# Kernel optimization log

Measured on AMD Instinct MI355X. Metric: run time of the kernel, lower is better.

The kernel has to match this reference:

```python
import jax, jax.numpy as jnp
import numpy as np

N = 262144
D = 6
M = 6
EPS = 1e-05
ALPHA = 0.05


def _w(k, out_dim, in_dim):
    # Kaiming-uniform-ish init like torch Linear default
    bound = 1.0 / np.sqrt(in_dim)
    return jax.random.uniform(k, (out_dim, in_dim), jnp.float32, -bound, bound)


def _b(k, out_dim, in_dim):
    bound = 1.0 / np.sqrt(in_dim)
    return jax.random.uniform(k, (out_dim,), jnp.float32, -bound, bound)


def setup_inputs() -> dict:
    key = jax.random.key(0)
    ks = jax.random.split(key, 32)
    inp = {
        "X": jax.random.normal(ks[0], (N, D), jnp.float32),
        "U": jax.random.normal(ks[1], (N, M), jnp.float32),
        "xref": jax.random.normal(ks[2], (1, D), jnp.float32),
        # FNN: 6 -> 80 -> 200 -> 6
        "fnn_w1": _w(ks[3], 80, D), "fnn_b1": _b(ks[4], 80, D),
        "fnn_w2": _w(ks[5], 200, 80), "fnn_b2": _b(ks[6], 200, 80),
        "fnn_w3": _w(ks[7], D, 200), "fnn_b3": _b(ks[8], D, 200),
        # GNN: 6 -> 36
        "gnn_w": _w(ks[9], D * M, D), "gnn_b": _b(ks[10], D * M, D),
        # ICNN: 6 -> 60 -> 60 -> 30 -> 1 with input skips
        "icnn_w1": _w(ks[11], 60, D), "icnn_b1": _b(ks[12], 60, D),
        "icnn_w2": _w(ks[13], 60, 60), "icnn_b2": _b(ks[14], 60, 60),
        "icnn_w3": _w(ks[15], 30, 60), "icnn_b3": _b(ks[16], 30, 60),
        "icnn_w4": _w(ks[17], 1, 30), "icnn_b4": _b(ks[18], 1, 30),
        "icnn_im2": _w(ks[19], 60, D),
        "icnn_im3": _w(ks[20], 30, D),
        "icnn_im4": _w(ks[21], 1, D),
    }
    return inp


def reference(X, U, xref,
              fnn_w1, fnn_b1, fnn_w2, fnn_b2, fnn_w3, fnn_b3,
              gnn_w, gnn_b,
              icnn_w1, icnn_b1, icnn_w2, icnn_b2, icnn_w3, icnn_b3,
              icnn_w4, icnn_b4, icnn_im2, icnn_im3, icnn_im4):
    def lin(x, W, b=None):
        y = x @ W.T
        return y if b is None else y + b

    def icnn(x):  # (n, D) -> (n, 1)
        h = jax.nn.softplus(lin(x, icnn_w1, icnn_b1))
        h = jax.nn.softplus(lin(h, icnn_w2, icnn_b2) + lin(x, icnn_im2))
        h = jax.nn.softplus(lin(h, icnn_w3, icnn_b3) + lin(x, icnn_im3))
        return lin(h, icnn_w4, icnn_b4) + lin(x, icnn_im4)

    def V_fn(Xb):  # (n, D) -> (n,)
        h = icnn(Xb)[:, 0] - icnn(xref)[0, 0]
        # sigma(h) = (h>=1)(h-0.5) + (0<h<1)(0.5 h^2)
        sigma = jnp.where(h >= 1.0, h - 0.5,
                          jnp.where(h > 0.0, 0.5 * h * h, 0.0))
        dx = Xb - xref
        return sigma + EPS * jnp.sum(dx * dx, axis=1)

    # FNN (tanh hiddens)
    h = jnp.tanh(lin(X, fnn_w1, fnn_b1))
    h = jnp.tanh(lin(h, fnn_w2, fnn_b2))
    f_X = lin(h, fnn_w3, fnn_b3)  # (N, D)

    # GNN
    g_X = lin(X, gnn_w, gnn_b).reshape(X.shape[0], D, M)  # (N, D, M)

    # Lyapunov value and its gradient (per-sample, via grad of summed V)
    V = V_fn(X)  # (N,)
    dV = jax.grad(lambda Z: jnp.sum(V_fn(Z)))(X)  # (N, D)

    # Stability correction
    sc = jnp.sum(dV * f_X, axis=1) + ALPHA * V
    sc = sc - jnp.sum(jnp.abs(jnp.einsum('nd,ndm->nm', dV, g_X)), axis=1)
    dV_norm = dV / jnp.sum(dV * dV, axis=1, keepdims=True)
    f_cor = -dV_norm * jax.nn.relu(sc)[:, None]

    dX_opt = f_X + f_cor + jnp.einsum('ndm,nm->nd', g_X, U)
    return dX_opt
```

## Files before the change

kernel.cpp:

```cpp
#include <hip/hip_runtime.h>

#define EPS 1e-05f
#define ALPHA 0.05f

typedef _Float16 h2v __attribute__((ext_vector_type(2)));
typedef _Float16 f16x8 __attribute__((ext_vector_type(8)));
typedef float f32x16 __attribute__((ext_vector_type(16)));

__device__ __forceinline__ float rcp_f(float x){ return __builtin_amdgcn_rcpf(x); }
__device__ __forceinline__ float dot2(h2v a, h2v b, float c){
  return __builtin_amdgcn_fdot2(a, b, c, false);
}
__device__ __forceinline__ h2v uh(uint u){ return __builtin_bit_cast(h2v, u); }
__device__ __forceinline__ float uf(uint u){ return __builtin_bit_cast(float, u); }

#define LOG2E 1.4426950408889634f
#define LN2   0.6931471805599453f

__device__ __forceinline__ float fast_tanh(float x){
  float ax = fabsf(x);
  float e  = exp2f(ax * (-2.0f * LOG2E));
  float t  = (1.0f - e) * rcp_f(1.0f + e);
  return copysignf(t, x);
}
__device__ __forceinline__ float fast_sp(float x){
  float ax = fabsf(x);
  float e  = exp2f(ax * -LOG2E);
  return fmaxf(x, 0.0f) + log2f(1.0f + e) * LN2;
}
__device__ __forceinline__ float fast_sig(float x){
  float ax = fabsf(x);
  float e  = exp2f(ax * -LOG2E);
  float r  = rcp_f(1.0f + e);
  return x >= 0.0f ? r : e * r;
}
__device__ __forceinline__ float sig_from_sp(float sp){
  return 1.0f - exp2f(sp * -LOG2E);
}
__device__ __forceinline__ h2v mkh2(float a, float b){
  h2v r; r.x = (_Float16)a; r.y = (_Float16)b; return r;
}
__device__ __forceinline__ uint packh(float a, float b){
  ushort lo = __builtin_bit_cast(ushort, (_Float16)a);
  ushort hi = __builtin_bit_cast(ushort, (_Float16)b);
  return (uint)lo | ((uint)hi << 16);
}

__global__ __launch_bounds__(512, 2) void holo_main(
    const float* __restrict__ X, const float* __restrict__ U,
    const float* __restrict__ xref,
    const float* __restrict__ fw1, const float* __restrict__ fb1,
    const float* __restrict__ fw2, const float* __restrict__ fb2,
    const float* __restrict__ fw3, const float* __restrict__ fb3,
    const float* __restrict__ gw,  const float* __restrict__ gb,
    const float* __restrict__ iw1, const float* __restrict__ ib1,
    const float* __restrict__ iw2, const float* __restrict__ ib2,
    const float* __restrict__ iw3, const float* __restrict__ ib3,
    const float* __restrict__ iw4, const float* __restrict__ ib4,
    const float* __restrict__ im2, const float* __restrict__ im3,
    const float* __restrict__ im4,
    float* __restrict__ out, int N)
{
  __shared__ alignas(16) ushort sW2r[224*84];
  __shared__ uint4 sW3E[224];
  __shared__ uint4 sPW1B[80];
  __shared__ uint4 sPGB[36];
  __shared__ uint4 sPI1B[60];
  __shared__ uint4 sPI1C[60];
  __shared__ uint4 sPI3[240];
  __shared__ uint4 sPI3C[240];
  __shared__ uint4 sPM2B[60];
  __shared__ uint4 sPM2C[60];
  __shared__ uint4 sPM3B[60];
  __shared__ uint4 sPM3C[30];
  __shared__ uint  sPM4u[4];
  __shared__ alignas(16) uint sPI2Tu[1800];
  __shared__ uint4 sPI2C[480];
  __shared__ float sFB3[6], sXREF[6], sIM4[6];
  __shared__ float sS1[60], sS2[60], sS3[30];
  __shared__ float sYREF, sIB4;

  const int t = threadIdx.x;
  const int T = 512;
  const int lane = t & 63;

  for (int idx=t; idx<224*42; idx+=T){
    int row = idx/42, c = idx%42, k = 2*c;
    uint v = 0;
    if (row < 200 && k < 80) v = packh(fw2[row*80+k], fw2[row*80+k+1]);
    ((uint*)sW2r)[idx] = v;
  }
  for (int idx=t; idx<896; idx+=T){
    int P = idx/8, c = idx%8, n = 2*P;
    uint v = 0;
    if (n < 200){
      if (c < 6)       v = packh(fw3[c*200+n], fw3[c*200+n+1]);
      else if (c == 6) v = __builtin_bit_cast(uint, fb2[n]);
      else             v = __builtin_bit_cast(uint, fb2[n+1]);
    }
    ((uint*)sW3E)[idx] = v;
  }
  for (int idx=t; idx<320; idx+=T){
    int o = idx/4, c = idx%4;
    ((uint*)sPW1B)[idx] = (c<3) ? packh(fw1[o*6+2*c], fw1[o*6+2*c+1])
                                : __builtin_bit_cast(uint, fb1[o]);
  }
  for (int idx=t; idx<144; idx+=T){
    int o = idx/4, c = idx%4;
    ((uint*)sPGB)[idx] = (c<3) ? packh(gw[o*6+2*c], gw[o*6+2*c+1])
                               : __builtin_bit_cast(uint, gb[o]);
  }
  for (int idx=t; idx<240; idx+=T){
    int p = idx/8, c = idx%8, sub = c/4, cc = c%4, nr = 2*p+sub;
    ((uint*)sPI1B)[idx] = (cc<3) ? packh(iw1[nr*6+2*cc], iw1[nr*6+2*cc+1])
                                 : __builtin_bit_cast(uint, ib1[nr]);
  }
  for (int idx=t; idx<240; idx+=T){
    int q = idx/8, c = idx%8;
    ((uint*)sPI1C)[idx] = (c<6) ? packh(iw1[(2*q)*6+c], iw1[(2*q+1)*6+c]) : 0u;
  }
  for (int idx=t; idx<960; idx+=T){
    int r = idx/32, q = idx%32;
    ((uint*)sPI3)[idx] = (q<30) ? packh(iw3[r*60+2*q], iw3[r*60+2*q+1]) : 0u;
  }
  for (int idx=t; idx<960; idx+=T){
    int j = idx/16, q = idx%16;
    ((uint*)sPI3C)[idx] = (q<15) ? packh(iw3[(2*q)*60+j], iw3[(2*q+1)*60+j]) : 0u;
  }
  for (int idx=t; idx<240; idx+=T){
    int j = idx/4, c = idx%4;
    ((uint*)sPM2B)[idx] = (c<3) ? packh(im2[j*6+2*c], im2[j*6+2*c+1])
                                : __builtin_bit_cast(uint, ib2[j]);
  }
  for (int idx=t; idx<240; idx+=T){
    int q = idx/8, c = idx%8;
    ((uint*)sPM2C)[idx] = (c<6) ? packh(im2[(2*q)*6+c], im2[(2*q+1)*6+c]) : 0u;
  }
  for (int idx=t; idx<240; idx+=T){
    int r = idx/8, c = idx%8;
    uint v = 0;
    if (c < 3)       v = packh(im3[r*6+2*c], im3[r*6+2*c+1]);
    else if (c == 3) v = __builtin_bit_cast(uint, ib3[r]);
    else if (c == 4) v = __builtin_bit_cast(uint, iw4[r]);
    ((uint*)sPM3B)[idx] = v;
  }
  for (int idx=t; idx<120; idx+=T){
    int q = idx/8, c = idx%8;
    ((uint*)sPM3C)[idx] = (c<6) ? packh(im3[(2*q)*6+c], im3[(2*q+1)*6+c]) : 0u;
  }
  for (int idx=t; idx<4; idx+=T)
    sPM4u[idx] = (idx<3) ? packh(im4[2*idx], im4[2*idx+1]) : 0u;
  for (int idx=t; idx<1800; idx+=T){
    int p = idx/60, j = idx%60;
    sPI2Tu[idx] = packh(iw2[j*60+2*p], iw2[j*60+2*p+1]);
  }
  for (int idx=t; idx<1920; idx+=T){
    int k1 = idx/32, q = idx%32;
    ((uint*)sPI2C)[idx] = (q<30) ? packh(iw2[(2*q)*60+k1], iw2[(2*q+1)*60+k1]) : 0u;
  }
  for (int k=t;k<6;k+=T){ sFB3[k]=fb3[k]; sIM4[k]=im4[k]; sXREF[k]=xref[k]; }
  if (t==0) sIB4=ib4[0];
  __syncthreads();

  {
    h2v xrp[3];
    #pragma unroll
    for (int p = 0; p < 3; p++) xrp[p] = mkh2(sXREF[2*p], sXREF[2*p+1]);
    if (t < 60){
      const uint* w = (const uint*)sPI1B + (t/2)*8 + (t&1)*4;
      float z = uf(w[3]);
      #pragma unroll
      for (int c = 0; c < 3; c++) z = dot2(uh(w[c]), xrp[c], z);
      sS1[t] = fast_sp(z);
    }
    __syncthreads();
    if (t < 60){
      const uint* m = (const uint*)sPM2B + t*4;
      float z = uf(m[3]);
      #pragma unroll
      for (int c = 0; c < 3; c++) z = dot2(uh(m[c]), xrp[c], z);
      for (int p = 0; p < 30; p++)
        z = dot2(uh(sPI2Tu[p*60+t]), mkh2(sS1[2*p], sS1[2*p+1]), z);
      sS2[t] = fast_sp(z);
    }
    __syncthreads();
    if (t < 30){
      const uint* m = (const uint*)sPM3B + t*8;
      float z = uf(m[3]);
      #pragma unroll
      for (int c = 0; c < 3; c++) z = dot2(uh(m[c]), xrp[c], z);
      const uint* prow = (const uint*)sPI3 + t*32;
      for (int q = 0; q < 30; q++)
        z = dot2(uh(prow[q]), mkh2(sS2[2*q], sS2[2*q+1]), z);
      sS3[t] = fast_sp(z);
    }
    __syncthreads();
    if (t == 0){
      float y = sIB4;
      #pragma unroll
      for (int p = 0; p < 3; p++) y = dot2(uh(sPM4u[p]), xrp[p], y);
      for (int j = 0; j < 30; j++) y = fmaf(uf(((const uint*)sPM3B)[j*8+4]), sS3[j], y);
      sYREF = y;
    }
    __syncthreads();
  }

  const int i = blockIdx.x * blockDim.x + t;
  const bool valid = (i < N);

  float x[6]; h2v xp[3];
  #pragma unroll
  for (int k = 0; k < 6; k++) x[k] = valid ? X[(long)i*6 + k] : 0.0f;
  #pragma unroll
  for (int p = 0; p < 3; p++) xp[p] = mkh2(x[2*p], x[2*p+1]);

  uint h1u[40];
  #pragma unroll
  for (int o = 0; o < 80; o += 2){
    uint4 wa = sPW1B[o], wb = sPW1B[o+1];
    float z0 = uf(wa.w), z1 = uf(wb.w);
    z0 = dot2(uh(wa.x), xp[0], z0); z0 = dot2(uh(wa.y), xp[1], z0); z0 = dot2(uh(wa.z), xp[2], z0);
    z1 = dot2(uh(wb.x), xp[0], z1); z1 = dot2(uh(wb.y), xp[1], z1); z1 = dot2(uh(wb.z), xp[2], z1);
    h1u[o/2] = packh(fast_tanh(z0), fast_tanh(z1));
  }

  const int hh = lane >> 5;
  const int l31 = lane & 31;

  uint bf0[5][4], bf1[5][4];
  {
    int a0 = 4 * l31;
    int a1 = 4 * (32 + l31);
    #pragma unroll
    for (int kt = 0; kt < 5; kt++){
      #pragma unroll
      for (int q = 0; q < 4; q++){
        int lo0 = __builtin_amdgcn_ds_bpermute(a0, (int)h1u[kt*8 + q]);
        int hi0 = __builtin_amdgcn_ds_bpermute(a0, (int)h1u[kt*8 + 4 + q]);
        bf0[kt][q] = hh ? (uint)hi0 : (uint)lo0;
        int lo1 = __builtin_amdgcn_ds_bpermute(a1, (int)h1u[kt*8 + q]);
        int hi1 = __builtin_amdgcn_ds_bpermute(a1, (int)h1u[kt*8 + 4 + q]);
        bf1[kt][q] = hh ? (uint)hi1 : (uint)lo1;
      }
    }
  }

  float fp0[6] = {0.f,0.f,0.f,0.f,0.f,0.f};
  float fp1[6] = {0.f,0.f,0.f,0.f,0.f,0.f};
  for (int mt = 0; mt < 7; mt++){
    const int row = mt*32 + l31;
    f16x8 af[5];
    #pragma unroll
    for (int kt = 0; kt < 5; kt++){
      const ushort* wp = &sW2r[row*84 + kt*16 + 8*hh];
      uint2 w0 = *(const uint2*)wp;
      uint2 w1 = *(const uint2*)(wp + 4);
      uint4 au; au.x = w0.x; au.y = w0.y; au.z = w1.x; au.w = w1.y;
      af[kt] = __builtin_bit_cast(f16x8, au);
    }
    f32x16 acc0 = {0,0,0,0,0,0,0,0,0,0,0,0,0,0,0,0};
    f32x16 acc1 = {0,0,0,0,0,0,0,0,0,0,0,0,0,0,0,0};
    #pragma unroll
    for (int kt = 0; kt < 5; kt++){
      uint4 b0u; b0u.x=bf0[kt][0]; b0u.y=bf0[kt][1]; b0u.z=bf0[kt][2]; b0u.w=bf0[kt][3];
      uint4 b1u; b1u.x=bf1[kt][0]; b1u.y=bf1[kt][1]; b1u.z=bf1[kt][2]; b1u.w=bf1[kt][3];
      acc0 = __builtin_amdgcn_mfma_f32_32x32x16_f16(af[kt], __builtin_bit_cast(f16x8, b0u), acc0, 0, 0, 0);
      acc1 = __builtin_amdgcn_mfma_f32_32x32x16_f16(af[kt], __builtin_bit_cast(f16x8, b1u), acc1, 0, 0, 0);
    }
    #pragma unroll
    for (int c = 0; c < 4; c++){
      #pragma unroll
      for (int b0h = 0; b0h < 2; b0h++){
        const int r0 = 4*c + 2*b0h;
        const int P  = mt*16 + 4*c + 2*hh + b0h;
        uint4 wa = sW3E[P*2], wb = sW3E[P*2+1];
        float bA = uf(wb.z), bB = uf(wb.w);
        h2v tp0 = mkh2(fast_tanh(acc0[r0] + bA), fast_tanh(acc0[r0+1] + bB));
        h2v tp1 = mkh2(fast_tanh(acc1[r0] + bA), fast_tanh(acc1[r0+1] + bB));
        fp0[0] = dot2(uh(wa.x), tp0, fp0[0]); fp1[0] = dot2(uh(wa.x), tp1, fp1[0]);
        fp0[1] = dot2(uh(wa.y), tp0, fp0[1]); fp1[1] = dot2(uh(wa.y), tp1, fp1[1]);
        fp0[2] = dot2(uh(wa.z), tp0, fp0[2]); fp1[2] = dot2(uh(wa.z), tp1, fp1[2]);
        fp0[3] = dot2(uh(wa.w), tp0, fp0[3]); fp1[3] = dot2(uh(wa.w), tp1, fp1[3]);
        fp0[4] = dot2(uh(wb.x), tp0, fp0[4]); fp1[4] = dot2(uh(wb.x), tp1, fp1[4]);
        fp0[5] = dot2(uh(wb.y), tp0, fp0[5]); fp1[5] = dot2(uh(wb.y), tp1, fp1[5]);
      }
    }
  }
  float f[6];
  #pragma unroll
  for (int d = 0; d < 6; d++){
    float s0 = fp0[d] + __shfl_xor(fp0[d], 32, 64);
    float s1 = fp1[d] + __shfl_xor(fp1[d], 32, 64);
    f[d] = sFB3[d] + (hh ? s1 : s0);
  }

  float c2[60];
  #pragma unroll
  for (int j = 0; j < 60; j++){
    uint4 m = sPM2B[j];
    float z = uf(m.w);
    z = dot2(uh(m.x), xp[0], z); z = dot2(uh(m.y), xp[1], z); z = dot2(uh(m.z), xp[2], z);
    c2[j] = z;
  }
  for (int p = 0; p < 30; p++){
    uint4 wA = sPI1B[2*p], wB = sPI1B[2*p+1];
    float za = uf(wA.w), zb = uf(wB.w);
    za = dot2(uh(wA.x), xp[0], za); za = dot2(uh(wA.y), xp[1], za); za = dot2(uh(wA.z), xp[2], za);
    zb = dot2(uh(wB.x), xp[0], zb); zb = dot2(uh(wB.y), xp[1], zb); zb = dot2(uh(wB.z), xp[2], zb);
    h2v s = mkh2(fast_sp(za), fast_sp(zb));
    const uint* rowp = sPI2Tu + p*60;
    #pragma unroll
    for (int jj = 0; jj < 15; jj++){
      uint4 v = *(const uint4*)(rowp + jj*4);
      c2[4*jj+0] = dot2(uh(v.x), s, c2[4*jj+0]);
      c2[4*jj+1] = dot2(uh(v.y), s, c2[4*jj+1]);
      c2[4*jj+2] = dot2(uh(v.z), s, c2[4*jj+2]);
      c2[4*jj+3] = dot2(uh(v.w), s, c2[4*jj+3]);
    }
  }
  h2v c2p[32];
  #pragma unroll
  for (int j = 0; j < 60; j += 2)
    c2p[j/2] = mkh2(fast_sp(c2[j]), fast_sp(c2[j+1]));
  c2p[30] = mkh2(0.f, 0.f); c2p[31] = mkh2(0.f, 0.f);

  float y = sIB4;
  #pragma unroll
  for (int p = 0; p < 3; p++) y = dot2(uh(sPM4u[p]), xp[p], y);
  float ac[6];
  #pragma unroll
  for (int d = 0; d < 6; d++) ac[d] = sIM4[d];
  float g3[30];
  #pragma unroll
  for (int i3 = 0; i3 < 30; i3++){
    uint4 m0 = sPM3B[2*i3], m1 = sPM3B[2*i3+1];
    float z = uf(m0.w);
    z = dot2(uh(m0.x), xp[0], z); z = dot2(uh(m0.y), xp[1], z); z = dot2(uh(m0.z), xp[2], z);
    const uint4* prow = sPI3 + i3*8;
    #pragma unroll
    for (int q4 = 0; q4 < 8; q4++){
      uint4 v = prow[q4];
      z = dot2(uh(v.x), c2p[4*q4+0], z);
      z = dot2(uh(v.y), c2p[4*q4+1], z);
      z = dot2(uh(v.z), c2p[4*q4+2], z);
      z = dot2(uh(v.w), c2p[4*q4+3], z);
    }
    float sp3 = fast_sp(z);
    float w4  = uf(m1.x);
    y = fmaf(w4, sp3, y);
    g3[i3] = w4 * sig_from_sp(sp3);
  }
  h2v g3p[16];
  #pragma unroll
  for (int q = 0; q < 15; q++) g3p[q] = mkh2(g3[2*q], g3[2*q+1]);
  g3p[15] = mkh2(0.f, 0.f);
  #pragma unroll
  for (int q = 0; q < 15; q++){
    uint4 a = sPM3C[2*q], b = sPM3C[2*q+1];
    ac[0] = dot2(uh(a.x), g3p[q], ac[0]);
    ac[1] = dot2(uh(a.y), g3p[q], ac[1]);
    ac[2] = dot2(uh(a.z), g3p[q], ac[2]);
    ac[3] = dot2(uh(a.w), g3p[q], ac[3]);
    ac[4] = dot2(uh(b.x), g3p[q], ac[4]);
    ac[5] = dot2(uh(b.y), g3p[q], ac[5]);
  }

  h2v g2p[32];
  #pragma unroll
  for (int jp = 0; jp < 30; jp++){
    const uint4* r0p = sPI3C + (2*jp)*4;
    const uint4* r1p = sPI3C + (2*jp+1)*4;
    float ta = 0.0f, tb = 0.0f;
    #pragma unroll
    for (int q4 = 0; q4 < 4; q4++){
      uint4 v0 = r0p[q4], v1 = r1p[q4];
      ta = dot2(uh(v0.x), g3p[4*q4+0], ta);
      ta = dot2(uh(v0.y), g3p[4*q4+1], ta);
      ta = dot2(uh(v0.z), g3p[4*q4+2], ta);
      ta = dot2(uh(v0.w), g3p[4*q4+3], ta);
      tb = dot2(uh(v1.x), g3p[4*q4+0], tb);
      tb = dot2(uh(v1.y), g3p[4*q4+1], tb);
      tb = dot2(uh(v1.z), g3p[4*q4+2], tb);
      tb = dot2(uh(v1.w), g3p[4*q4+3], tb);
    }
    h2v sp = c2p[jp];
    ta *= sig_from_sp((float)sp.x);
    tb *= sig_from_sp((float)sp.y);
    h2v tp = mkh2(ta, tb);
    g2p[jp] = tp;
    uint4 a = sPM2C[2*jp], b = sPM2C[2*jp+1];
    ac[0] = dot2(uh(a.x), tp, ac[0]);
    ac[1] = dot2(uh(a.y), tp, ac[1]);
    ac[2] = dot2(uh(a.z), tp, ac[2]);
    ac[3] = dot2(uh(a.w), tp, ac[3]);
    ac[4] = dot2(uh(b.x), tp, ac[4]);
    ac[5] = dot2(uh(b.y), tp, ac[5]);
  }
  g2p[30] = mkh2(0.f, 0.f); g2p[31] = mkh2(0.f, 0.f);

  for (int p = 0; p < 30; p++){
    uint4 wA = sPI1B[2*p], wB = sPI1B[2*p+1];
    float za = uf(wA.w), zb = uf(wB.w);
    za = dot2(uh(wA.x), xp[0], za); za = dot2(uh(wA.y), xp[1], za); za = dot2(uh(wA.z), xp[2], za);
    zb = dot2(uh(wB.x), xp[0], zb); zb = dot2(uh(wB.y), xp[1], zb); zb = dot2(uh(wB.z), xp[2], zb);
    const uint4* c0 = sPI2C + (2*p)*8;
    const uint4* c1 = sPI2C + (2*p+1)*8;
    float ta = 0.0f, tb = 0.0f;
    #pragma unroll
    for (int q4 = 0; q4 < 8; q4++){
      uint4 v0 = c0[q4], v1 = c1[q4];
      ta = dot2(uh(v0.x), g2p[4*q4+0], ta);
      ta = dot2(uh(v0.y), g2p[4*q4+1], ta);
      ta = dot2(uh(v0.z), g2p[4*q4+2], ta);
      ta = dot2(uh(v0.w), g2p[4*q4+3], ta);
      tb = dot2(uh(v1.x), g2p[4*q4+0], tb);
      tb = dot2(uh(v1.y), g2p[4*q4+1], tb);
      tb = dot2(uh(v1.z), g2p[4*q4+2], tb);
      tb = dot2(uh(v1.w), g2p[4*q4+3], tb);
    }
    ta *= fast_sig(za); tb *= fast_sig(zb);
    h2v tp = mkh2(ta, tb);
    uint4 a = sPI1C[2*p], b = sPI1C[2*p+1];
    ac[0] = dot2(uh(a.x), tp, ac[0]);
    ac[1] = dot2(uh(a.y), tp, ac[1]);
    ac[2] = dot2(uh(a.z), tp, ac[2]);
    ac[3] = dot2(uh(a.w), tp, ac[3]);
    ac[4] = dot2(uh(b.x), tp, ac[4]);
    ac[5] = dot2(uh(b.y), tp, ac[5]);
  }

  float hdiff = y - sYREF;
  float sigma = (hdiff >= 1.0f) ? (hdiff - 0.5f) : ((hdiff > 0.0f) ? 0.5f*hdiff*hdiff : 0.0f);
  float sigp  = (hdiff >= 1.0f) ? 1.0f          : ((hdiff > 0.0f) ? hdiff             : 0.0f);
  float dx2 = 0.0f;
  float dV[6];
  #pragma unroll
  for (int d = 0; d < 6; d++){
    float dx = x[d] - sXREF[d];
    dx2 = fmaf(dx, dx, dx2);
    dV[d] = fmaf(sigp, ac[d], 2.0f*EPS*dx);
  }
  float V = sigma + EPS*dx2;

  float sc = ALPHA * V;
  #pragma unroll
  for (int d = 0; d < 6; d++) sc = fmaf(dV[d], f[d], sc);

  float u[6];
  #pragma unroll
  for (int m = 0; m < 6; m++) u[m] = valid ? U[(long)i*6 + m] : 0.0f;
  float am[6] = {0.f,0.f,0.f,0.f,0.f,0.f};
  float gU[6];
  #pragma unroll
  for (int d = 0; d < 6; d++){
    float acc = 0.0f;
    #pragma unroll
    for (int m = 0; m < 6; m++){
      int o = d*6 + m;
      uint4 g4 = sPGB[o];
      float g = uf(g4.w);
      g = dot2(uh(g4.x), xp[0], g); g = dot2(uh(g4.y), xp[1], g); g = dot2(uh(g4.z), xp[2], g);
      am[m] = fmaf(dV[d], g, am[m]);
      acc   = fmaf(g, u[m], acc);
    }
    gU[d] = acc;
  }
  #pragma unroll
  for (int m = 0; m < 6; m++) sc -= fabsf(am[m]);

  float n2 = 0.0f;
  #pragma unroll
  for (int d = 0; d < 6; d++) n2 = fmaf(dV[d], dV[d], n2);
  float r = fmaxf(sc, 0.0f) * rcp_f(n2);

  if (valid){
    #pragma unroll
    for (int d = 0; d < 6; d++)
      out[(long)i*6 + d] = f[d] - dV[d]*r + gU[d];
  }
}

extern "C" void kernel_launch(void* const* d_in, const int* in_sizes, int n_in,
                              void* d_out, int out_size, void* d_ws, size_t ws_size,
                              hipStream_t stream)
{
  const float* X    = (const float*)d_in[0];
  const float* U    = (const float*)d_in[1];
  const float* xref = (const float*)d_in[2];
  const float* fw1  = (const float*)d_in[3];
  const float* fb1  = (const float*)d_in[4];
  const float* fw2  = (const float*)d_in[5];
  const float* fb2  = (const float*)d_in[6];
  const float* fw3  = (const float*)d_in[7];
  const float* fb3  = (const float*)d_in[8];
  const float* gw   = (const float*)d_in[9];
  const float* gb   = (const float*)d_in[10];
  const float* iw1  = (const float*)d_in[11];
  const float* ib1  = (const float*)d_in[12];
  const float* iw2  = (const float*)d_in[13];
  const float* ib2  = (const float*)d_in[14];
  const float* iw3  = (const float*)d_in[15];
  const float* ib3  = (const float*)d_in[16];
  const float* iw4  = (const float*)d_in[17];
  const float* ib4  = (const float*)d_in[18];
  const float* im2  = (const float*)d_in[19];
  const float* im3  = (const float*)d_in[20];
  const float* im4  = (const float*)d_in[21];

  float* out = (float*)d_out;
  int N = in_sizes[0] / 6;

  int threads = 512;
  int blocks  = (N + threads - 1) / threads;
  holo_main<<<blocks, threads, 0, stream>>>(X, U, xref,
      fw1, fb1, fw2, fb2, fw3, fb3, gw, gb,
      iw1, ib1, iw2, ib2, iw3, ib3, iw4, ib4, im2, im3, im4,
      out, N);
}
```

Before: 198.3 us.

## Move packed ICNN/GNN weights to constant memory via a prep kernel

Adds a single-block prep kernel that packs most small weight tables and computes the xref ICNN value once, then copies them device-to-device into a __constant__ buffer. The main kernel reads these uniform weights from constant memory (scalar loads) instead of staging them into LDS in every block. This removes per-block global loads, packing and barriers, and shrinks LDS use. The cost is an extra kernel launch, a memcpy on the stream, and more scalar-load pressure and register use in the main kernel. It also skips a few dead W3 iterations.

```diff
diff --git a/kernel.cpp b/kernel.cpp
--- a/kernel.cpp
+++ b/kernel.cpp
@@ -46,43 +46,168 @@
   return (uint)lo | ((uint)hi << 16);
 }
 
-__global__ __launch_bounds__(512, 2) void holo_main(
-    const float* __restrict__ X, const float* __restrict__ U,
+static constexpr int O_PW1B = 0;
+static constexpr int O_PGB  = 320;
+static constexpr int O_PI1B = 464;
+static constexpr int O_PI1C = 704;
+static constexpr int O_PI3  = 944;
+static constexpr int O_PI3C = 1904;
+static constexpr int O_PM2B = 2928;
+static constexpr int O_PM2C = 3184;
+static constexpr int O_PM3B = 3440;
+static constexpr int O_PM3C = 3680;
+static constexpr int O_PM4  = 3800;
+static constexpr int O_FB3  = 3804;
+static constexpr int O_XREF = 3810;
+static constexpr int O_IM4  = 3816;
+static constexpr int O_IB4  = 3822;
+static constexpr int O_YREF = 3823;
+static constexpr int O_PI2T = 3824;
+static constexpr int O_PI2C = 5624;
+static constexpr int W_TOTAL = 7544;
+
+__device__ uint g_stage[W_TOTAL];
+__constant__ uint cW[W_TOTAL];
+
+__global__ void holo_prep(
     const float* __restrict__ xref,
     const float* __restrict__ fw1, const float* __restrict__ fb1,
-    const float* __restrict__ fw2, const float* __restrict__ fb2,
-    const float* __restrict__ fw3, const float* __restrict__ fb3,
+    const float* __restrict__ fb3,
     const float* __restrict__ gw,  const float* __restrict__ gb,
     const float* __restrict__ iw1, const float* __restrict__ ib1,
     const float* __restrict__ iw2, const float* __restrict__ ib2,
     const float* __restrict__ iw3, const float* __restrict__ ib3,
     const float* __restrict__ iw4, const float* __restrict__ ib4,
     const float* __restrict__ im2, const float* __restrict__ im3,
-    const float* __restrict__ im4,
+    const float* __restrict__ im4)
+{
+  uint* gs = g_stage;
+  const int t = threadIdx.x, T = 256;
+  __shared__ float sS1[60], sS2[60], sS3[30];
+
+  for (int idx=t; idx<320; idx+=T){
+    int o = idx/4, c = idx%4;
+    gs[O_PW1B+idx] = (c<3) ? packh(fw1[o*6+2*c], fw1[o*6+2*c+1])
+                           : __builtin_bit_cast(uint, fb1[o]);
+  }
+  for (int idx=t; idx<144; idx+=T){
+    int o = idx/4, c = idx%4;
+    gs[O_PGB+idx] = (c<3) ? packh(gw[o*6+2*c], gw[o*6+2*c+1])
+                          : __builtin_bit_cast(uint, gb[o]);
+  }
+  for (int idx=t; idx<240; idx+=T){
+    int p = idx/8, c = idx%8, sub = c/4, cc = c%4, nr = 2*p+sub;
+    gs[O_PI1B+idx] = (cc<3) ? packh(iw1[nr*6+2*cc], iw1[nr*6+2*cc+1])
+                            : __builtin_bit_cast(uint, ib1[nr]);
+  }
+  for (int idx=t; idx<240; idx+=T){
+    int q = idx/8, c = idx%8;
+    gs[O_PI1C+idx] = (c<6) ? packh(iw1[(2*q)*6+c], iw1[(2*q+1)*6+c]) : 0u;
+  }
+  for (int idx=t; idx<960; idx+=T){
+    int r = idx/32, q = idx%32;
+    gs[O_PI3+idx] = (q<30) ? packh(iw3[r*60+2*q], iw3[r*60+2*q+1]) : 0u;
+  }
+  for (int idx=t; idx<1024; idx+=T){
+    int j = idx/16, q = idx%16;
+    gs[O_PI3C+idx] = (j<60 && q<15) ? packh(iw3[(2*q)*60+j], iw3[(2*q+1)*60+j]) : 0u;
+  }
+  for (int idx=t; idx<256; idx+=T){
+    int j = idx/4, c = idx%4;
+    uint v = 0;
+    if (j < 60) v = (c<3) ? packh(im2[j*6+2*c], im2[j*6+2*c+1])
+                          : __builtin_bit_cast(uint, ib2[j]);
+    gs[O_PM2B+idx] = v;
+  }
+  for (int idx=t; idx<256; idx+=T){
+    int q = idx/8, c = idx%8;
+    gs[O_PM2C+idx] = (q<30 && c<6) ? packh(im2[(2*q)*6+c], im2[(2*q+1)*6+c]) : 0u;
+  }
+  for (int idx=t; idx<240; idx+=T){
+    int r = idx/8, c = idx%8;
+    uint v = 0;
+    if (c < 3)       v = packh(im3[r*6+2*c], im3[r*6+2*c+1]);
+    else if (c == 3) v = __builtin_bit_cast(uint, ib3[r]);
+    else if (c == 4) v = __builtin_bit_cast(uint, iw4[r]);
+    gs[O_PM3B+idx] = v;
+  }
+  for (int idx=t; idx<120; idx+=T){
+    int q = idx/8, c = idx%8;
+    gs[O_PM3C+idx] = (c<6) ? packh(im3[(2*q)*6+c], im3[(2*q+1)*6+c]) : 0u;
+  }
+  for (int idx=t; idx<4; idx+=T)
+    gs[O_PM4+idx] = (idx<3) ? packh(im4[2*idx], im4[2*idx+1]) : 0u;
+  for (int k=t; k<6; k+=T){
+    gs[O_FB3+k]  = __builtin_bit_cast(uint, fb3[k]);
+    gs[O_XREF+k] = __builtin_bit_cast(uint, xref[k]);
+    gs[O_IM4+k]  = __builtin_bit_cast(uint, im4[k]);
+  }
+  if (t==0) gs[O_IB4] = __builtin_bit_cast(uint, ib4[0]);
+  for (int idx=t; idx<1800; idx+=T){
+    int p = idx/60, j = idx%60;
+    gs[O_PI2T+idx] = packh(iw2[j*60+2*p], iw2[j*60+2*p+1]);
+  }
+  for (int idx=t; idx<1920; idx+=T){
+    int k1 = idx/32, q = idx%32;
+    gs[O_PI2C+idx] = (q<30) ? packh(iw2[(2*q)*60+k1], iw2[(2*q+1)*60+k1]) : 0u;
+  }
+  __threadfence_block();
+  __syncthreads();
+
+  h2v xrp[3];
+  #pragma unroll
+  for (int p = 0; p < 3; p++) xrp[p] = mkh2(xref[2*p], xref[2*p+1]);
+  if (t < 60){
+    const uint* w = gs + O_PI1B + (t/2)*8 + (t&1)*4;
+    float z = uf(w[3]);
+    #pragma unroll
+    for (int c = 0; c < 3; c++) z = dot2(uh(w[c]), xrp[c], z);
+    sS1[t] = fast_sp(z);
+  }
+  __syncthreads();
+  if (t < 60){
+    const uint* m = gs + O_PM2B + t*4;
+    float z = uf(m[3]);
+    #pragma unroll
+    for (int c = 0; c < 3; c++) z = dot2(uh(m[c]), xrp[c], z);
+    for (int p = 0; p < 30; p++)
+      z = dot2(uh(gs[O_PI2T + p*60 + t]), mkh2(sS1[2*p], sS1[2*p+1]), z);
+    sS2[t] = fast_sp(z);
+  }
+  __syncthreads();
+  if (t < 30){
+    const uint* m = gs + O_PM3B + t*8;
+    float z = uf(m[3]);
+    #pragma unroll
+    for (int c = 0; c < 3; c++) z = dot2(uh(m[c]), xrp[c], z);
+    for (int q = 0; q < 30; q++)
+      z = dot2(uh(gs[O_PI3 + t*32 + q]), mkh2(sS2[2*q], sS2[2*q+1]), z);
+    sS3[t] = fast_sp(z);
+  }
+  __syncthreads();
+  if (t == 0){
+    float y = uf(gs[O_IB4]);
+    #pragma unroll
+    for (int p = 0; p < 3; p++) y = dot2(uh(gs[O_PM4+p]), xrp[p], y);
+    for (int j = 0; j < 30; j++) y = fmaf(uf(gs[O_PM3B+j*8+4]), sS3[j], y);
+    gs[O_YREF] = __builtin_bit_cast(uint, y);
+  }
+}
+
+__global__ __launch_bounds__(512, 2) void holo_main(
+    const float* __restrict__ X, const float* __restrict__ U,
+    const float* __restrict__ fw2, const float* __restrict__ fb2,
+    const float* __restrict__ fw3,
     float* __restrict__ out, int N)
 {
   __shared__ alignas(16) ushort sW2r[224*84];
   __shared__ uint4 sW3E[224];
-  __shared__ uint4 sPW1B[80];
-  __shared__ uint4 sPGB[36];
-  __shared__ uint4 sPI1B[60];
-  __shared__ uint4 sPI1C[60];
-  __shared__ uint4 sPI3[240];
-  __shared__ uint4 sPI3C[240];
-  __shared__ uint4 sPM2B[60];
-  __shared__ uint4 sPM2C[60];
-  __shared__ uint4 sPM3B[60];
-  __shared__ uint4 sPM3C[30];
-  __shared__ uint  sPM4u[4];
-  __shared__ alignas(16) uint sPI2Tu[1800];
-  __shared__ uint4 sPI2C[480];
-  __shared__ float sFB3[6], sXREF[6], sIM4[6];
-  __shared__ float sS1[60], sS2[60], sS3[30];
-  __shared__ float sYREF, sIB4;
 
   const int t = threadIdx.x;
   const int T = 512;
   const int lane = t & 63;
+  const int hh  = lane >> 5;
+  const int l31 = lane & 31;
 
   for (int idx=t; idx<224*42; idx+=T){
     int row = idx/42, c = idx%42, k = 2*c;
@@ -100,110 +225,7 @@
     }
     ((uint*)sW3E)[idx] = v;
   }
-  for (int idx=t; idx<320; idx+=T){
-    int o = idx/4, c = idx%4;
-    ((uint*)sPW1B)[idx] = (c<3) ? packh(fw1[o*6+2*c], fw1[o*6+2*c+1])
-                                : __builtin_bit_cast(uint, fb1[o]);
-  }
-  for (int idx=t; idx<144; idx+=T){
-    int o = idx/4, c = idx%4;
-    ((uint*)sPGB)[idx] = (c<3) ? packh(gw[o*6+2*c], gw[o*6+2*c+1])
-                               : __builtin_bit_cast(uint, gb[o]);
-  }
-  for (int idx=t; idx<240; idx+=T){
-    int p = idx/8, c = idx%8, sub = c/4, cc = c%4, nr = 2*p+sub;
-    ((uint*)sPI1B)[idx] = (cc<3) ? packh(iw1[nr*6+2*cc], iw1[nr*6+2*cc+1])
-                                 : __builtin_bit_cast(uint, ib1[nr]);
-  }
-  for (int idx=t; idx<240; idx+=T){
-    int q = idx/8, c = idx%8;
-    ((uint*)sPI1C)[idx] = (c<6) ? packh(iw1[(2*q)*6+c], iw1[(2*q+1)*6+c]) : 0u;
-  }
-  for (int idx=t; idx<960; idx+=T){
-    int r = idx/32, q = idx%32;
-    ((uint*)sPI3)[idx] = (q<30) ? packh(iw3[r*60+2*q], iw3[r*60+2*q+1]) : 0u;
-  }
-  for (int idx=t; idx<960; idx+=T){
-    int j = idx/16, q = idx%16;
-    ((uint*)sPI3C)[idx] = (q<15) ? packh(iw3[(2*q)*60+j], iw3[(2*q+1)*60+j]) : 0u;
-  }
-  for (int idx=t; idx<240; idx+=T){
-    int j = idx/4, c = idx%4;
-    ((uint*)sPM2B)[idx] = (c<3) ? packh(im2[j*6+2*c], im2[j*6+2*c+1])
-                                : __builtin_bit_cast(uint, ib2[j]);
-  }
-  for (int idx=t; idx<240; idx+=T){
-    int q = idx/8, c = idx%8;
-    ((uint*)sPM2C)[idx] = (c<6) ? packh(im2[(2*q)*6+c], im2[(2*q+1)*6+c]) : 0u;
-  }
-  for (int idx=t; idx<240; idx+=T){
-    int r = idx/8, c = idx%8;
-    uint v = 0;
-    if (c < 3)       v = packh(im3[r*6+2*c], im3[r*6+2*c+1]);
-    else if (c == 3) v = __builtin_bit_cast(uint, ib3[r]);
-    else if (c == 4) v = __builtin_bit_cast(uint, iw4[r]);
-    ((uint*)sPM3B)[idx] = v;
-  }
-  for (int idx=t; idx<120; idx+=T){
-    int q = idx/8, c = idx%8;
-    ((uint*)sPM3C)[idx] = (c<6) ? packh(im3[(2*q)*6+c], im3[(2*q+1)*6+c]) : 0u;
-  }
-  for (int idx=t; idx<4; idx+=T)
-    sPM4u[idx] = (idx<3) ? packh(im4[2*idx], im4[2*idx+1]) : 0u;
-  for (int idx=t; idx<1800; idx+=T){
-    int p = idx/60, j = idx%60;
-    sPI2Tu[idx] = packh(iw2[j*60+2*p], iw2[j*60+2*p+1]);
-  }
-  for (int idx=t; idx<1920; idx+=T){
-    int k1 = idx/32, q = idx%32;
-    ((uint*)sPI2C)[idx] = (q<30) ? packh(iw2[(2*q)*60+k1], iw2[(2*q+1)*60+k1]) : 0u;
-  }
-  for (int k=t;k<6;k+=T){ sFB3[k]=fb3[k]; sIM4[k]=im4[k]; sXREF[k]=xref[k]; }
-  if (t==0) sIB4=ib4[0];
   __syncthreads();
-
-  {
-    h2v xrp[3];
-    #pragma unroll
-    for (int p = 0; p < 3; p++) xrp[p] = mkh2(sXREF[2*p], sXREF[2*p+1]);
-    if (t < 60){
-      const uint* w = (const uint*)sPI1B + (t/2)*8 + (t&1)*4;
-      float z = uf(w[3]);
-      #pragma unroll
-      for (int c = 0; c < 3; c++) z = dot2(uh(w[c]), xrp[c], z);
-      sS1[t] = fast_sp(z);
-    }
-    __syncthreads();
-    if (t < 60){
-      const uint* m = (const uint*)sPM2B + t*4;
-      float z = uf(m[3]);
-      #pragma unroll
-      for (int c = 0; c < 3; c++) z = dot2(uh(m[c]), xrp[c], z);
-      for (int p = 0; p < 30; p++)
-        z = dot2(uh(sPI2Tu[p*60+t]), mkh2(sS1[2*p], sS1[2*p+1]), z);
-      sS2[t] = fast_sp(z);
-    }
-    __syncthreads();
-    if (t < 30){
-      const uint* m = (const uint*)sPM3B + t*8;
-      float z = uf(m[3]);
-      #pragma unroll
-      for (int c = 0; c < 3; c++) z = dot2(uh(m[c]), xrp[c], z);
-      const uint* prow = (const uint*)sPI3 + t*32;
-      for (int q = 0; q < 30; q++)
-        z = dot2(uh(prow[q]), mkh2(sS2[2*q], sS2[2*q+1]), z);
-      sS3[t] = fast_sp(z);
-    }
-    __syncthreads();
-    if (t == 0){
-      float y = sIB4;
-      #pragma unroll
-      for (int p = 0; p < 3; p++) y = dot2(uh(sPM4u[p]), xrp[p], y);
-      for (int j = 0; j < 30; j++) y = fmaf(uf(((const uint*)sPM3B)[j*8+4]), sS3[j], y);
-      sYREF = y;
-    }
-    __syncthreads();
-  }
 
   const int i = blockIdx.x * blockDim.x + t;
   const bool valid = (i < N);
@@ -217,15 +239,14 @@
   uint h1u[40];
   #pragma unroll
   for (int o = 0; o < 80; o += 2){
-    uint4 wa = sPW1B[o], wb = sPW1B[o+1];
-    float z0 = uf(wa.w), z1 = uf(wb.w);
-    z0 = dot2(uh(wa.x), xp[0], z0); z0 = dot2(uh(wa.y), xp[1], z0); z0 = dot2(uh(wa.z), xp[2], z0);
-    z1 = dot2(uh(wb.x), xp[0], z1); z1 = dot2(uh(wb.y), xp[1], z1); z1 = dot2(uh(wb.z), xp[2], z1);
+    float z0 = uf(cW[O_PW1B + o*4 + 3]), z1 = uf(cW[O_PW1B + (o+1)*4 + 3]);
+    #pragma unroll
+    for (int c = 0; c < 3; c++){
+      z0 = dot2(uh(cW[O_PW1B + o*4 + c]),     xp[c], z0);
+      z1 = dot2(uh(cW[O_PW1B + (o+1)*4 + c]), xp[c], z1);
+    }
     h1u[o/2] = packh(fast_tanh(z0), fast_tanh(z1));
   }
-
-  const int hh = lane >> 5;
-  const int l31 = lane & 31;
 
   uint bf0[5][4], bf1[5][4];
   {
@@ -271,6 +292,7 @@
     for (int c = 0; c < 4; c++){
       #pragma unroll
       for (int b0h = 0; b0h < 2; b0h++){
+        if (mt == 6 && c > 0) continue;
         const int r0 = 4*c + 2*b0h;
         const int P  = mt*16 + 4*c + 2*hh + b0h;
         uint4 wa = sW3E[P*2], wb = sW3E[P*2+1];
@@ -291,152 +313,114 @@
   for (int d = 0; d < 6; d++){
     float s0 = fp0[d] + __shfl_xor(fp0[d], 32, 64);
     float s1 = fp1[d] + __shfl_xor(fp1[d], 32, 64);
-    f[d] = sFB3[d] + (hh ? s1 : s0);
+    f[d] = uf(cW[O_FB3+d]) + (hh ? s1 : s0);
   }
 
   float c2[60];
   #pragma unroll
   for (int j = 0; j < 60; j++){
-    uint4 m = sPM2B[j];
-    float z = uf(m.w);
-    z = dot2(uh(m.x), xp[0], z); z = dot2(uh(m.y), xp[1], z); z = dot2(uh(m.z), xp[2], z);
+    float z = uf(cW[O_PM2B + j*4 + 3]);
+    z = dot2(uh(cW[O_PM2B+j*4+0]), xp[0], z);
+    z = dot2(uh(cW[O_PM2B+j*4+1]), xp[1], z);
+    z = dot2(uh(cW[O_PM2B+j*4+2]), xp[2], z);
     c2[j] = z;
   }
   for (int p = 0; p < 30; p++){
-    uint4 wA = sPI1B[2*p], wB = sPI1B[2*p+1];
-    float za = uf(wA.w), zb = uf(wB.w);
-    za = dot2(uh(wA.x), xp[0], za); za = dot2(uh(wA.y), xp[1], za); za = dot2(uh(wA.z), xp[2], za);
-    zb = dot2(uh(wB.x), xp[0], zb); zb = dot2(uh(wB.y), xp[1], zb); zb = dot2(uh(wB.z), xp[2], zb);
+    float za = uf(cW[O_PI1B + p*8 + 3]);
+    float zb = uf(cW[O_PI1B + p*8 + 7]);
+    #pragma unroll
+    for (int c = 0; c < 3; c++){
+      za = dot2(uh(cW[O_PI1B + p*8 + c]),     xp[c], za);
+      zb = dot2(uh(cW[O_PI1B + p*8 + 4 + c]), xp[c], zb);
+    }
     h2v s = mkh2(fast_sp(za), fast_sp(zb));
-    const uint* rowp = sPI2Tu + p*60;
-    #pragma unroll
-    for (int jj = 0; jj < 15; jj++){
-      uint4 v = *(const uint4*)(rowp + jj*4);
-      c2[4*jj+0] = dot2(uh(v.x), s, c2[4*jj+0]);
-      c2[4*jj+1] = dot2(uh(v.y), s, c2[4*jj+1]);
-      c2[4*jj+2] = dot2(uh(v.z), s, c2[4*jj+2]);
-      c2[4*jj+3] = dot2(uh(v.w), s, c2[4*jj+3]);
-    }
-  }
-  h2v c2p[32];
+    #pragma unroll
+    for (int j = 0; j < 60; j++)
+      c2[j] = dot2(uh(cW[O_PI2T + p*60 + j]), s, c2[j]);
+  }
+  h2v c2p[30];
   #pragma unroll
   for (int j = 0; j < 60; j += 2)
     c2p[j/2] = mkh2(fast_sp(c2[j]), fast_sp(c2[j+1]));
-  c2p[30] = mkh2(0.f, 0.f); c2p[31] = mkh2(0.f, 0.f);
-
-  float y = sIB4;
-  #pragma unroll
-  for (int p = 0; p < 3; p++) y = dot2(uh(sPM4u[p]), xp[p], y);
+
+  float y = uf(cW[O_IB4]);
+  #pragma unroll
+  for (int p = 0; p < 3; p++) y = dot2(uh(cW[O_PM4+p]), xp[p], y);
   float ac[6];
   #pragma unroll
-  for (int d = 0; d < 6; d++) ac[d] = sIM4[d];
-  float g3[30];
+  for (int d = 0; d < 6; d++) ac[d] = uf(cW[O_IM4+d]);
+  h2v g3p[15];
+  float g3even;
   #pragma unroll
   for (int i3 = 0; i3 < 30; i3++){
-    uint4 m0 = sPM3B[2*i3], m1 = sPM3B[2*i3+1];
-    float z = uf(m0.w);
-    z = dot2(uh(m0.x), xp[0], z); z = dot2(uh(m0.y), xp[1], z); z = dot2(uh(m0.z), xp[2], z);
-    const uint4* prow = sPI3 + i3*8;
-    #pragma unroll
-    for (int q4 = 0; q4 < 8; q4++){
-      uint4 v = prow[q4];
-      z = dot2(uh(v.x), c2p[4*q4+0], z);
-      z = dot2(uh(v.y), c2p[4*q4+1], z);
-      z = dot2(uh(v.z), c2p[4*q4+2], z);
-      z = dot2(uh(v.w), c2p[4*q4+3], z);
-    }
+    float z = uf(cW[O_PM3B + i3*8 + 3]);
+    z = dot2(uh(cW[O_PM3B+i3*8+0]), xp[0], z);
+    z = dot2(uh(cW[O_PM3B+i3*8+1]), xp[1], z);
+    z = dot2(uh(cW[O_PM3B+i3*8+2]), xp[2], z);
+    #pragma unroll
+    for (int q = 0; q < 30; q++)
+      z = dot2(uh(cW[O_PI3 + i3*32 + q]), c2p[q], z);
     float sp3 = fast_sp(z);
-    float w4  = uf(m1.x);
+    float w4  = uf(cW[O_PM3B + i3*8 + 4]);
     y = fmaf(w4, sp3, y);
-    g3[i3] = w4 * sig_from_sp(sp3);
-  }
-  h2v g3p[16];
-  #pragma unroll
-  for (int q = 0; q < 15; q++) g3p[q] = mkh2(g3[2*q], g3[2*q+1]);
-  g3p[15] = mkh2(0.f, 0.f);
+    float gi = w4 * sig_from_sp(sp3);
+    if (i3 & 1) g3p[i3>>1] = mkh2(g3even, gi); else g3even = gi;
+  }
   #pragma unroll
   for (int q = 0; q < 15; q++){
-    uint4 a = sPM3C[2*q], b = sPM3C[2*q+1];
-    ac[0] = dot2(uh(a.x), g3p[q], ac[0]);
-    ac[1] = dot2(uh(a.y), g3p[q], ac[1]);
-    ac[2] = dot2(uh(a.z), g3p[q], ac[2]);
-    ac[3] = dot2(uh(a.w), g3p[q], ac[3]);
-    ac[4] = dot2(uh(b.x), g3p[q], ac[4]);
-    ac[5] = dot2(uh(b.y), g3p[q], ac[5]);
-  }
-
-  h2v g2p[32];
+    #pragma unroll
+    for (int d = 0; d < 6; d++)
+      ac[d] = dot2(uh(cW[O_PM3C + q*8 + d]), g3p[q], ac[d]);
+  }
+
+  h2v g2p[30];
   #pragma unroll
   for (int jp = 0; jp < 30; jp++){
-    const uint4* r0p = sPI3C + (2*jp)*4;
-    const uint4* r1p = sPI3C + (2*jp+1)*4;
     float ta = 0.0f, tb = 0.0f;
     #pragma unroll
-    for (int q4 = 0; q4 < 4; q4++){
-      uint4 v0 = r0p[q4], v1 = r1p[q4];
-      ta = dot2(uh(v0.x), g3p[4*q4+0], ta);
-      ta = dot2(uh(v0.y), g3p[4*q4+1], ta);
-      ta = dot2(uh(v0.z), g3p[4*q4+2], ta);
-      ta = dot2(uh(v0.w), g3p[4*q4+3], ta);
-      tb = dot2(uh(v1.x), g3p[4*q4+0], tb);
-      tb = dot2(uh(v1.y), g3p[4*q4+1], tb);
-      tb = dot2(uh(v1.z), g3p[4*q4+2], tb);
-      tb = dot2(uh(v1.w), g3p[4*q4+3], tb);
+    for (int q = 0; q < 15; q++){
+      ta = dot2(uh(cW[O_PI3C + (2*jp)*16 + q]),   g3p[q], ta);
+      tb = dot2(uh(cW[O_PI3C + (2*jp+1)*16 + q]), g3p[q], tb);
     }
     h2v sp = c2p[jp];
     ta *= sig_from_sp((float)sp.x);
     tb *= sig_from_sp((float)sp.y);
     h2v tp = mkh2(ta, tb);
     g2p[jp] = tp;
-    uint4 a = sPM2C[2*jp], b = sPM2C[2*jp+1];
-    ac[0] = dot2(uh(a.x), tp, ac[0]);
-    ac[1] = dot2(uh(a.y), tp, ac[1]);
-    ac[2] = dot2(uh(a.z), tp, ac[2]);
-    ac[3] = dot2(uh(a.w), tp, ac[3]);
-    ac[4] = dot2(uh(b.x), tp, ac[4]);
-    ac[5] = dot2(uh(b.y), tp, ac[5]);
-  }
-  g2p[30] = mkh2(0.f, 0.f); g2p[31] = mkh2(0.f, 0.f);
+    #pragma unroll
+    for (int d = 0; d < 6; d++)
+      ac[d] = dot2(uh(cW[O_PM2C + jp*8 + d]), tp, ac[d]);
+  }
 
   for (int p = 0; p < 30; p++){
-    uint4 wA = sPI1B[2*p], wB = sPI1B[2*p+1];
-    float za = uf(wA.w), zb = uf(wB.w);
-    za = dot2(uh(wA.x), xp[0], za); za = dot2(uh(wA.y), xp[1], za); za = dot2(uh(wA.z), xp[2], za);
-    zb = dot2(uh(wB.x), xp[0], zb); zb = dot2(uh(wB.y), xp[1], zb); zb = dot2(uh(wB.z), xp[2], zb);
-    const uint4* c0 = sPI2C + (2*p)*8;
-    const uint4* c1 = sPI2C + (2*p+1)*8;
+    float za = uf(cW[O_PI1B + p*8 + 3]);
+    float zb = uf(cW[O_PI1B + p*8 + 7]);
+    #pragma unroll
+    for (int c = 0; c < 3; c++){
+      za = dot2(uh(cW[O_PI1B + p*8 + c]),     xp[c], za);
+      zb = dot2(uh(cW[O_PI1B + p*8 + 4 + c]), xp[c], zb);
+    }
     float ta = 0.0f, tb = 0.0f;
     #pragma unroll
-    for (int q4 = 0; q4 < 8; q4++){
-      uint4 v0 = c0[q4], v1 = c1[q4];
-      ta = dot2(uh(v0.x), g2p[4*q4+0], ta);
-      ta = dot2(uh(v0.y), g2p[4*q4+1], ta);
-      ta = dot2(uh(v0.z), g2p[4*q4+2], ta);
-      ta = dot2(uh(v0.w), g2p[4*q4+3], ta);
-      tb = dot2(uh(v1.x), g2p[4*q4+0], tb);
-      tb = dot2(uh(v1.y), g2p[4*q4+1], tb);
-      tb = dot2(uh(v1.z), g2p[4*q4+2], tb);
-      tb = dot2(uh(v1.w), g2p[4*q4+3], tb);
+    for (int q = 0; q < 30; q++){
+      ta = dot2(uh(cW[O_PI2C + (2*p)*32 + q]),   g2p[q], ta);
+      tb = dot2(uh(cW[O_PI2C + (2*p+1)*32 + q]), g2p[q], tb);
     }
     ta *= fast_sig(za); tb *= fast_sig(zb);
     h2v tp = mkh2(ta, tb);
-    uint4 a = sPI1C[2*p], b = sPI1C[2*p+1];
-    ac[0] = dot2(uh(a.x), tp, ac[0]);
-    ac[1] = dot2(uh(a.y), tp, ac[1]);
-    ac[2] = dot2(uh(a.z), tp, ac[2]);
-    ac[3] = dot2(uh(a.w), tp, ac[3]);
-    ac[4] = dot2(uh(b.x), tp, ac[4]);
-    ac[5] = dot2(uh(b.y), tp, ac[5]);
-  }
-
-  float hdiff = y - sYREF;
+    #pragma unroll
+    for (int d = 0; d < 6; d++)
+      ac[d] = dot2(uh(cW[O_PI1C + p*8 + d]), tp, ac[d]);
+  }
+
+  float hdiff = y - uf(cW[O_YREF]);
   float sigma = (hdiff >= 1.0f) ? (hdiff - 0.5f) : ((hdiff > 0.0f) ? 0.5f*hdiff*hdiff : 0.0f);
   float sigp  = (hdiff >= 1.0f) ? 1.0f          : ((hdiff > 0.0f) ? hdiff             : 0.0f);
   float dx2 = 0.0f;
   float dV[6];
   #pragma unroll
   for (int d = 0; d < 6; d++){
-    float dx = x[d] - sXREF[d];
+    float dx = x[d] - uf(cW[O_XREF+d]);
     dx2 = fmaf(dx, dx, dx2);
     dV[d] = fmaf(sigp, ac[d], 2.0f*EPS*dx);
   }
@@ -457,9 +441,10 @@
     #pragma unroll
     for (int m = 0; m < 6; m++){
       int o = d*6 + m;
-      uint4 g4 = sPGB[o];
-      float g = uf(g4.w);
-      g = dot2(uh(g4.x), xp[0], g); g = dot2(uh(g4.y), xp[1], g); g = dot2(uh(g4.z), xp[2], g);
+      float g = uf(cW[O_PGB + o*4 + 3]);
+      g = dot2(uh(cW[O_PGB+o*4+0]), xp[0], g);
+      g = dot2(uh(cW[O_PGB+o*4+1]), xp[1], g);
+      g = dot2(uh(cW[O_PGB+o*4+2]), xp[2], g);
       am[m] = fmaf(dV[d], g, am[m]);
       acc   = fmaf(g, u[m], acc);
     }
@@ -510,10 +495,18 @@
   float* out = (float*)d_out;
   int N = in_sizes[0] / 6;
 
+  holo_prep<<<1, 256, 0, stream>>>(xref, fw1, fb1, fb3, gw, gb,
+                                   iw1, ib1, iw2, ib2, iw3, ib3,
+                                   iw4, ib4, im2, im3, im4);
+
+  void* stage_ptr = nullptr;
+  void* const_ptr = nullptr;
+  hipGetSymbolAddress(&stage_ptr, HIP_SYMBOL(g_stage));
+  hipGetSymbolAddress(&const_ptr, HIP_SYMBOL(cW));
+  hipMemcpyAsync(const_ptr, stage_ptr, W_TOTAL * sizeof(uint),
+                 hipMemcpyDeviceToDevice, stream);
+
   int threads = 512;
   int blocks  = (N + threads - 1) / threads;
-  holo_main<<<blocks, threads, 0, stream>>>(X, U, xref,
-      fw1, fb1, fw2, fb2, fw3, fb3, gw, gb,
-      iw1, ib1, iw2, ib2, iw3, ib3, iw4, ib4, im2, im3, im4,
-      out, N);
-}
+  holo_main<<<blocks, threads, 0, stream>>>(X, U, fw2, fb2, fw3, out, N);
+}
```

New measurement: 236.7 us. 19.4% more time.
